# Kernel optimization log

Hardware: AMD Instinct MI355X
Metric: run time of the kernel (lower is better)

## Reference

```python
import jax, jax.numpy as jnp
import numpy as np

CAPACITY = 1024


def setup_inputs() -> dict:
    T, H, I, E, K = 2048, 1024, 1408, 8, 2
    key = jax.random.key(0)
    k0, k1, k2, k3, k4 = jax.random.split(key, 5)
    hidden_states = jax.random.normal(k0, (T, H), dtype=jnp.float32)
    w1 = jax.random.normal(k1, (E, 2 * I, H), dtype=jnp.float32) * 0.02  # [gate; up]
    w2 = jax.random.normal(k2, (E, H, I), dtype=jnp.float32) * 0.02
    topk_weights = jax.random.uniform(k3, (T, K), dtype=jnp.float32)
    topk_ids = jax.random.randint(k4, (T, K), 0, E, dtype=jnp.int32)
    return {"hidden_states": hidden_states, "w1": w1, "w2": w2,
            "topk_weights": topk_weights, "topk_ids": topk_ids}


def reference(hidden_states, w1, w2, topk_weights, topk_ids):
    # MoE: prepare(dispatch) -> grouped expert GEMM (silu-gated MLP) -> finalize(combine)
    T, H = hidden_states.shape
    E = w1.shape[0]
    I = w2.shape[2]
    K = topk_ids.shape[1]
    C = CAPACITY

    # ---- prepare: dispatch token copies to per-expert buffers ----
    flat_ids = topk_ids.reshape(-1)                       # (T*K,)
    onehot = jax.nn.one_hot(flat_ids, E, dtype=jnp.int32)  # (T*K, E)
    cs = jnp.cumsum(onehot, axis=0)                        # running per-expert counts
    pos = jnp.take_along_axis(cs, flat_ids[:, None], axis=1)[:, 0] - 1  # slot in expert buffer
    keep = pos < C
    pos_c = jnp.where(keep, pos, 0)

    x_flat = jnp.repeat(hidden_states, K, axis=0)          # (T*K, H)
    x_e = jnp.zeros((E, C, H), dtype=hidden_states.dtype)
    x_e = x_e.at[flat_ids, pos_c].add(jnp.where(keep[:, None], x_flat, 0.0))

    # ---- grouped expert GEMM: silu(gate) * up, then down-proj ----
    h = jnp.einsum('ech,eoh->eco', x_e, w1)                # (E, C, 2I)
    gate, up = h[..., :I], h[..., I:]
    act = jax.nn.silu(gate) * up                           # (E, C, I)
    y = jnp.einsum('eci,ehi->ech', act, w2)                # (E, C, H)

    # ---- finalize: gather back, apply router weights, reduce over top-k ----
    y_flat = y[flat_ids, pos_c] * (keep[:, None].astype(y.dtype)) \
             * topk_weights.reshape(-1, 1)                 # (T*K, H)
    out = y_flat.reshape(T, K, H).sum(axis=1)              # (T, H)
    return out.astype(hidden_states.dtype)
```

## Files before the change

kernel.cpp:

```cpp
#include <hip/hip_runtime.h>

#define NE 8
#define CAP 1024
#define HD 1024
#define ID 1408
#define TT 2048

typedef __attribute__((ext_vector_type(8))) short bf16x8;
typedef __attribute__((ext_vector_type(4))) float f32x4;
typedef unsigned short u16;
typedef unsigned int u32;
typedef unsigned long long u64;

__device__ __forceinline__ u16 f2bf(float f) {
  u32 u = __float_as_uint(f);
  u = (u + 0x7fffu + ((u >> 16) & 1u)) >> 16;
  return (u16)u;
}

__device__ __forceinline__ bf16x8 pack8(float4 a, float4 b) {
  bf16x8 r;
  r[0] = (short)f2bf(a.x); r[1] = (short)f2bf(a.y);
  r[2] = (short)f2bf(a.z); r[3] = (short)f2bf(a.w);
  r[4] = (short)f2bf(b.x); r[5] = (short)f2bf(b.y);
  r[6] = (short)f2bf(b.z); r[7] = (short)f2bf(b.w);
  return r;
}

__device__ __forceinline__ void async_cp16(const void* g, void* l) {
  __builtin_amdgcn_global_load_lds(
      (const __attribute__((address_space(1))) u32*)g,
      (__attribute__((address_space(3))) u32*)l, 16, 0, 0);
}

#define W1B (NE * 2 * ID / 4)
#define W2B (NE * HD * ID / 4096)
#define XB (TT * HD / 4096)
__global__ __launch_bounds__(256) void prep_kernel(
    const float4* __restrict__ w1, bf16x8* __restrict__ bw1,
    const float4* __restrict__ w2, bf16x8* __restrict__ bw2,
    const float4* __restrict__ x, bf16x8* __restrict__ bx,
    float4* __restrict__ out, const int* __restrict__ ids,
    int* __restrict__ rowmap, int* __restrict__ counts) {
  int b = blockIdx.x;
  int tid = threadIdx.x;
  if (b == 0) {
    __shared__ unsigned char ids_s[TT * 2];
    __shared__ int sc[256][NE + 1];
    for (int i = tid; i < TT * 2; i += 256) ids_s[i] = (unsigned char)ids[i];
    __syncthreads();
    int base = tid * 16;
    u64 own64 = 0;
#pragma unroll
    for (int j = 0; j < 16; ++j) own64 += 1ull << (ids_s[base + j] * 8);
    int own[NE];
#pragma unroll
    for (int e = 0; e < NE; ++e) {
      own[e] = (int)((own64 >> (e * 8)) & 0xff);
      sc[tid][e] = own[e];
    }
    __syncthreads();
    for (int off = 1; off < 256; off <<= 1) {
      int v[NE];
      if (tid >= off) {
#pragma unroll
        for (int e = 0; e < NE; ++e) v[e] = sc[tid - off][e];
      }
      __syncthreads();
      if (tid >= off) {
#pragma unroll
        for (int e = 0; e < NE; ++e) sc[tid][e] += v[e];
      }
      __syncthreads();
    }
    if (tid == 255) {
#pragma unroll
      for (int e = 0; e < NE; ++e) counts[e] = sc[255][e] < CAP ? sc[255][e] : CAP;
    }
    int excl[NE];
#pragma unroll
    for (int e = 0; e < NE; ++e) excl[e] = sc[tid][e] - own[e];
    __syncthreads();
#pragma unroll
    for (int e = 0; e < NE; ++e) sc[tid][e] = excl[e];
#pragma unroll
    for (int j = 0; j < 16; ++j) {
      int f = base + j;
      int e = ids_s[f];
      int p = sc[tid][e]++;
      if (p < CAP) rowmap[e * CAP + p] = f;
    }
    return;
  }
  int bb = b - 1;
  if (bb < W1B) {
    int rl = tid >> 6, c = tid & 63;
    int g = bb * 4 + rl;
    int e = g / (2 * ID);
    int n = g - e * (2 * ID);
    int j = (n < ID) ? n : (n - ID);
    int np = (j >> 4) * 32 + (j & 15) + ((n < ID) ? 0 : 16);
    const float4* src = w1 + ((size_t)e * 2 * ID + n) * (HD / 4);
    bf16x8* dst = bw1 + ((size_t)e * 2 * ID + np) * (HD / 8);
    float4 v0 = src[c * 2];
    float4 v1 = src[c * 2 + 1];
    float4 v2 = src[128 + c * 2];
    float4 v3 = src[128 + c * 2 + 1];
    dst[c] = pack8(v0, v1);
    dst[64 + c] = pack8(v2, v3);
  } else if (bb < W1B + W2B) {
    size_t base4 = (size_t)(bb - W1B) * 1024;
    float4 v0 = w2[base4 + tid * 2];
    float4 v1 = w2[base4 + tid * 2 + 1];
    float4 v2 = w2[base4 + 512 + tid * 2];
    float4 v3 = w2[base4 + 512 + tid * 2 + 1];
    bf16x8* dst = bw2 + base4 / 2;
    dst[tid] = pack8(v0, v1);
    dst[256 + tid] = pack8(v2, v3);
  } else {
    size_t base4 = (size_t)(bb - W1B - W2B) * 1024;
    float4 v0 = x[base4 + tid * 2];
    float4 v1 = x[base4 + tid * 2 + 1];
    float4 v2 = x[base4 + 512 + tid * 2];
    float4 v3 = x[base4 + 512 + tid * 2 + 1];
    bf16x8* dst = bx + base4 / 2;
    dst[tid] = pack8(v0, v1);
    dst[256 + tid] = pack8(v2, v3);
    float4 z = {0.f, 0.f, 0.f, 0.f};
    out[base4 + tid] = z;
    out[base4 + 256 + tid] = z;
    out[base4 + 512 + tid] = z;
    out[base4 + 768 + tid] = z;
  }
}

#define G1BUF 24576
__global__ __launch_bounds__(256) void gemm1_kernel(
    const u16* __restrict__ A, const u16* __restrict__ B, u16* __restrict__ Hb,
    const int* __restrict__ rowmap, const int* __restrict__ counts) {
  int e = blockIdx.x;
  int count = counts[e];
  int m0 = blockIdx.y * 64;
  if (m0 >= count) return;
  int n0 = blockIdx.z * 128;
  int tid = threadIdx.x;
  int lane = tid & 63, wid = tid >> 6;
  int wm = wid >> 1, wn = wid & 1;
  int q = lane >> 4, lm = lane & 15;

  __shared__ __align__(16) char sm[3 * G1BUF];

  int rloc = tid >> 3;
  int chs = ((tid & 7) ^ (rloc & 7)) * 8;
  const u16* aP[2];
  const u16* bP[4];
#pragma unroll
  for (int i = 0; i < 2; ++i) {
    int gr = m0 + rloc + 32 * i;
    int f = (gr < count) ? rowmap[e * CAP + gr] : 0;
    aP[i] = A + (size_t)(f >> 1) * HD + chs;
  }
#pragma unroll
  for (int i = 0; i < 4; ++i)
    bP[i] = B + ((size_t)e * 2 * ID + n0 + rloc + 32 * i) * HD + chs;

  f32x4 zero = {0.f, 0.f, 0.f, 0.f};
  f32x4 acc[2][4];
#pragma unroll
  for (int mi = 0; mi < 2; ++mi)
#pragma unroll
    for (int ni = 0; ni < 4; ++ni) acc[mi][ni] = zero;

#define STAGE1(base, kt)                                             \
  do {                                                               \
    int ko_ = (kt) * 64;                                             \
    char* sb_ = (base);                                              \
    async_cp16(aP[0] + ko_, sb_ + (0 * 256 + tid) * 16);             \
    async_cp16(aP[1] + ko_, sb_ + (1 * 256 + tid) * 16);             \
    async_cp16(bP[0] + ko_, sb_ + 8192 + (0 * 256 + tid) * 16);      \
    async_cp16(bP[1] + ko_, sb_ + 8192 + (1 * 256 + tid) * 16);      \
    async_cp16(bP[2] + ko_, sb_ + 8192 + (2 * 256 + tid) * 16);      \
    async_cp16(bP[3] + ko_, sb_ + 8192 + (3 * 256 + tid) * 16);      \
  } while (0)

  STAGE1(sm, 0);
  STAGE1(sm + G1BUF, 1);
  int p = 0, pn2 = 2;
  for (int kt = 0; kt < HD / 64; ++kt) {
    if (kt == HD / 64 - 1)
      asm volatile("s_waitcnt vmcnt(0)\ns_barrier" ::: "memory");
    else
      asm volatile("s_waitcnt vmcnt(6)\ns_barrier" ::: "memory");
    const char* sb = sm + p * G1BUF;
    if (kt + 2 < HD / 64) STAGE1(sm + pn2 * G1BUF, kt + 2);
#pragma unroll
    for (int s = 0; s < 2; ++s) {
      int cs = ((s * 4 + q) ^ (lm & 7)) * 16;
      bf16x8 af[2], bfr[4];
#pragma unroll
      for (int mi = 0; mi < 2; ++mi)
        af[mi] = *(const bf16x8*)(sb + (wm * 32 + mi * 16 + lm) * 128 + cs);
#pragma unroll
      for (int ni = 0; ni < 4; ++ni)
        bfr[ni] = *(const bf16x8*)(sb + 8192 + (wn * 64 + ni * 16 + lm) * 128 + cs);
      __builtin_amdgcn_s_setprio(1);
#pragma unroll
      for (int mi = 0; mi < 2; ++mi)
#pragma unroll
        for (int ni = 0; ni < 4; ++ni)
          acc[mi][ni] = __builtin_amdgcn_mfma_f32_16x16x32_bf16(af[mi], bfr[ni], acc[mi][ni], 0, 0, 0);
      __builtin_amdgcn_s_setprio(0);
    }
    p = (p == 2) ? 0 : p + 1;
    pn2 = (pn2 == 2) ? 0 : pn2 + 1;
  }
  __syncthreads();

  u16* smOut = (u16*)sm;
#pragma unroll
  for (int mi = 0; mi < 2; ++mi) {
#pragma unroll
    for (int k = 0; k < 2; ++k) {
      int colL = wn * 32 + k * 16 + lm;
#pragma unroll
      for (int r = 0; r < 4; ++r) {
        float g = acc[mi][2 * k][r];
        float u = acc[mi][2 * k + 1][r];
        float a = g / (1.f + __expf(-g)) * u;
        int row = wm * 32 + mi * 16 + q * 4 + r;
        smOut[row * 72 + colL] = f2bf(a);
      }
    }
  }
  __syncthreads();
  {
    int row = tid >> 2, seg = tid & 3;
    const u16* sp = smOut + row * 72 + seg * 16;
    bf16x8 v0 = *(const bf16x8*)sp;
    bf16x8 v1 = *(const bf16x8*)(sp + 8);
    u16* dp = Hb + ((size_t)e * CAP + m0 + row) * ID + (n0 >> 1) + seg * 16;
    *(bf16x8*)dp = v0;
    *(bf16x8*)(dp + 8) = v1;
  }
}

#define G2BUF 16384
__global__ __launch_bounds__(256) void gemm2_kernel(
    const u16* __restrict__ A, const u16* __restrict__ B, float* __restrict__ out,
    const int* __restrict__ rowmap, const int* __restrict__ counts,
    const float* __restrict__ tw) {
  int e = blockIdx.x;
  int count = counts[e];
  int m0 = blockIdx.y * 64;
  if (m0 >= count) return;
  int n0 = blockIdx.z * 64;
  int tid = threadIdx.x;
  int lane = tid & 63, wid = tid >> 6;
  int wm = wid >> 1, wn = wid & 1;
  int q = lane >> 4, lm = lane & 15;

  __shared__ __align__(16) char sm[3 * G2BUF];

  int rloc = tid >> 3;
  int chs = ((tid & 7) ^ (rloc & 7)) * 8;
  const u16* aP[2];
  const u16* bP[2];
#pragma unroll
  for (int i = 0; i < 2; ++i) {
    aP[i] = A + ((size_t)e * CAP + m0 + rloc + 32 * i) * ID + chs;
    bP[i] = B + ((size_t)e * HD + n0 + rloc + 32 * i) * ID + chs;
  }

  f32x4 zero = {0.f, 0.f, 0.f, 0.f};
  f32x4 acc[2][2];
#pragma unroll
  for (int mi = 0; mi < 2; ++mi)
#pragma unroll
    for (int ni = 0; ni < 2; ++ni) acc[mi][ni] = zero;

#define STAGE2(base, kt)                                             \
  do {                                                               \
    int ko_ = (kt) * 64;                                             \
    char* sb_ = (base);                                              \
    async_cp16(aP[0] + ko_, sb_ + (0 * 256 + tid) * 16);             \
    async_cp16(aP[1] + ko_, sb_ + (1 * 256 + tid) * 16);             \
    async_cp16(bP[0] + ko_, sb_ + 8192 + (0 * 256 + tid) * 16);      \
    async_cp16(bP[1] + ko_, sb_ + 8192 + (1 * 256 + tid) * 16);      \
  } while (0)

  STAGE2(sm, 0);
  STAGE2(sm + G2BUF, 1);
  int p = 0, pn2 = 2;
  for (int kt = 0; kt < ID / 64; ++kt) {
    if (kt == ID / 64 - 1)
      asm volatile("s_waitcnt vmcnt(0)\ns_barrier" ::: "memory");
    else
      asm volatile("s_waitcnt vmcnt(4)\ns_barrier" ::: "memory");
    const char* sb = sm + p * G2BUF;
    if (kt + 2 < ID / 64) STAGE2(sm + pn2 * G2BUF, kt + 2);
#pragma unroll
    for (int s = 0; s < 2; ++s) {
      int cs = ((s * 4 + q) ^ (lm & 7)) * 16;
      bf16x8 af[2], bfr[2];
#pragma unroll
      for (int mi = 0; mi < 2; ++mi)
        af[mi] = *(const bf16x8*)(sb + (wm * 32 + mi * 16 + lm) * 128 + cs);
#pragma unroll
      for (int ni = 0; ni < 2; ++ni)
        bfr[ni] = *(const bf16x8*)(sb + 8192 + (wn * 32 + ni * 16 + lm) * 128 + cs);
      __builtin_amdgcn_s_setprio(1);
#pragma unroll
      for (int mi = 0; mi < 2; ++mi)
#pragma unroll
        for (int ni = 0; ni < 2; ++ni)
          acc[mi][ni] = __builtin_amdgcn_mfma_f32_16x16x32_bf16(af[mi], bfr[ni], acc[mi][ni], 0, 0, 0);
      __builtin_amdgcn_s_setprio(0);
    }
    p = (p == 2) ? 0 : p + 1;
    pn2 = (pn2 == 2) ? 0 : pn2 + 1;
  }

#pragma unroll
  for (int mi = 0; mi < 2; ++mi) {
#pragma unroll
    for (int r = 0; r < 4; ++r) {
      int grow = m0 + wm * 32 + mi * 16 + q * 4 + r;
      if (grow < count) {
        int f = rowmap[e * CAP + grow];
        float w = tw[f];
        int t = f >> 1;
#pragma unroll
        for (int ni = 0; ni < 2; ++ni) {
          int col = n0 + wn * 32 + ni * 16 + lm;
          atomicAdd(&out[(size_t)t * HD + col], w * acc[mi][ni][r]);
        }
      }
    }
  }
}

extern "C" void kernel_launch(void* const* d_in, const int* in_sizes, int n_in,
                              void* d_out, int out_size, void* d_ws, size_t ws_size,
                              hipStream_t stream) {
  const float* hidden = (const float*)d_in[0];
  const float* w1 = (const float*)d_in[1];
  const float* w2 = (const float*)d_in[2];
  const float* tw = (const float*)d_in[3];
  const int* ids = (const int*)d_in[4];
  float* out = (float*)d_out;

  char* p = (char*)d_ws;
  auto alloc = [&](size_t b) { char* r = p; p += (b + 255) & ~(size_t)255; return r; };
  u16* bw1 = (u16*)alloc((size_t)NE * 2 * ID * HD * 2);
  u16* bw2 = (u16*)alloc((size_t)NE * HD * ID * 2);
  u16* bx = (u16*)alloc((size_t)TT * HD * 2);
  u16* hbuf = (u16*)alloc((size_t)NE * CAP * ID * 2);
  int* rowmap = (int*)alloc((size_t)NE * CAP * 4);
  int* counts = (int*)alloc((size_t)NE * 4);

  prep_kernel<<<1 + W1B + W2B + XB, 256, 0, stream>>>(
      (const float4*)w1, (bf16x8*)bw1, (const float4*)w2, (bf16x8*)bw2,
      (const float4*)hidden, (bf16x8*)bx, (float4*)out, ids, rowmap, counts);

  gemm1_kernel<<<dim3(NE, CAP / 64, 2 * ID / 128), 256, 0, stream>>>(
      bx, bw1, hbuf, rowmap, counts);

  gemm2_kernel<<<dim3(NE, CAP / 64, HD / 64), 256, 0, stream>>>(
      hbuf, bw2, out, rowmap, counts, tw);
}
```

Before: 262.3 us.

## Move w2 conversion and output zeroing into gemm1 launch to overlap with GEMM

The w2 fp32-to-bf16 conversion and the output zeroing move out of the prep kernel and into extra leading blocks of the gemm1 launch. That work then runs alongside the first GEMM instead of before it. The prep kernel now converts w1 and x with one row (or one 256-element chunk) per block using 4-wide stores, giving more, smaller blocks. The extra blocks in gemm1 compete with GEMM blocks for CUs, and the narrower stores in prep may lower bandwidth efficiency.

Result: faster. 256.7 us (-2.1%).

```diff
diff --git a/kernel.cpp b/kernel.cpp
--- a/kernel.cpp
+++ b/kernel.cpp
@@ -33,15 +33,13 @@
       (__attribute__((address_space(3))) u32*)l, 16, 0, 0);
 }
 
-#define W1B (NE * 2 * ID / 4)
-#define W2B (NE * HD * ID / 4096)
-#define XB (TT * HD / 4096)
+#define W1ROWS (NE * 2 * ID)
+#define XBLK (TT * HD / 4 / 256)
 __global__ __launch_bounds__(256) void prep_kernel(
-    const float4* __restrict__ w1, bf16x8* __restrict__ bw1,
-    const float4* __restrict__ w2, bf16x8* __restrict__ bw2,
-    const float4* __restrict__ x, bf16x8* __restrict__ bx,
-    float4* __restrict__ out, const int* __restrict__ ids,
-    int* __restrict__ rowmap, int* __restrict__ counts) {
+    const float4* __restrict__ w1, ushort4* __restrict__ bw1,
+    const float4* __restrict__ x, ushort4* __restrict__ bx,
+    const int* __restrict__ ids, int* __restrict__ rowmap,
+    int* __restrict__ counts) {
   int b = blockIdx.x;
   int tid = threadIdx.x;
   if (b == 0) {
@@ -93,57 +91,59 @@
     return;
   }
   int bb = b - 1;
-  if (bb < W1B) {
-    int rl = tid >> 6, c = tid & 63;
-    int g = bb * 4 + rl;
-    int e = g / (2 * ID);
-    int n = g - e * (2 * ID);
+  if (bb < W1ROWS) {
+    int n = bb % (2 * ID);
+    int e = bb / (2 * ID);
     int j = (n < ID) ? n : (n - ID);
     int np = (j >> 4) * 32 + (j & 15) + ((n < ID) ? 0 : 16);
-    const float4* src = w1 + ((size_t)e * 2 * ID + n) * (HD / 4);
-    bf16x8* dst = bw1 + ((size_t)e * 2 * ID + np) * (HD / 8);
-    float4 v0 = src[c * 2];
-    float4 v1 = src[c * 2 + 1];
-    float4 v2 = src[128 + c * 2];
-    float4 v3 = src[128 + c * 2 + 1];
-    dst[c] = pack8(v0, v1);
-    dst[64 + c] = pack8(v2, v3);
-  } else if (bb < W1B + W2B) {
-    size_t base4 = (size_t)(bb - W1B) * 1024;
-    float4 v0 = w2[base4 + tid * 2];
-    float4 v1 = w2[base4 + tid * 2 + 1];
-    float4 v2 = w2[base4 + 512 + tid * 2];
-    float4 v3 = w2[base4 + 512 + tid * 2 + 1];
-    bf16x8* dst = bw2 + base4 / 2;
-    dst[tid] = pack8(v0, v1);
-    dst[256 + tid] = pack8(v2, v3);
+    float4 v = w1[((size_t)e * 2 * ID + n) * (HD / 4) + tid];
+    ushort4 o;
+    o.x = f2bf(v.x); o.y = f2bf(v.y); o.z = f2bf(v.z); o.w = f2bf(v.w);
+    bw1[((size_t)e * 2 * ID + np) * (HD / 4) + tid] = o;
   } else {
-    size_t base4 = (size_t)(bb - W1B - W2B) * 1024;
-    float4 v0 = x[base4 + tid * 2];
-    float4 v1 = x[base4 + tid * 2 + 1];
-    float4 v2 = x[base4 + 512 + tid * 2];
-    float4 v3 = x[base4 + 512 + tid * 2 + 1];
-    bf16x8* dst = bx + base4 / 2;
-    dst[tid] = pack8(v0, v1);
-    dst[256 + tid] = pack8(v2, v3);
-    float4 z = {0.f, 0.f, 0.f, 0.f};
-    out[base4 + tid] = z;
-    out[base4 + 256 + tid] = z;
-    out[base4 + 512 + tid] = z;
-    out[base4 + 768 + tid] = z;
+    size_t i = (size_t)(bb - W1ROWS) * 256 + tid;
+    float4 v = x[i];
+    ushort4 o;
+    o.x = f2bf(v.x); o.y = f2bf(v.y); o.z = f2bf(v.z); o.w = f2bf(v.w);
+    bx[i] = o;
   }
 }
 
 #define G1BUF 24576
 __global__ __launch_bounds__(256) void gemm1_kernel(
     const u16* __restrict__ A, const u16* __restrict__ B, u16* __restrict__ Hb,
-    const int* __restrict__ rowmap, const int* __restrict__ counts) {
-  int e = blockIdx.x;
+    const int* __restrict__ rowmap, const int* __restrict__ counts,
+    const float4* __restrict__ W2, bf16x8* __restrict__ bw2,
+    float4* __restrict__ outz) {
+  int bid = blockIdx.x;
+  int tid = threadIdx.x;
+  if (bid < 704) {
+#pragma unroll
+    for (int k2 = 0; k2 < 4; ++k2) {
+      size_t base4 = ((size_t)bid * 4 + k2) * 1024;
+      float4 v0 = W2[base4 + tid * 2];
+      float4 v1 = W2[base4 + tid * 2 + 1];
+      float4 v2 = W2[base4 + 512 + tid * 2];
+      float4 v3 = W2[base4 + 512 + tid * 2 + 1];
+      bf16x8* dst = bw2 + base4 / 2;
+      dst[tid] = pack8(v0, v1);
+      dst[256 + tid] = pack8(v2, v3);
+    }
+    return;
+  }
+  if (bid < 768) {
+    size_t base = (size_t)(bid - 704) * 8192;
+    float4 z = {0.f, 0.f, 0.f, 0.f};
+#pragma unroll
+    for (int i2 = 0; i2 < 32; ++i2) outz[base + i2 * 256 + tid] = z;
+    return;
+  }
+  int g = bid - 768;
+  int e = g & 7;
+  int m0 = ((g >> 3) & 15) * 64;
+  int n0 = (g >> 7) * 128;
   int count = counts[e];
-  int m0 = blockIdx.y * 64;
   if (m0 >= count) return;
-  int n0 = blockIdx.z * 128;
-  int tid = threadIdx.x;
   int lane = tid & 63, wid = tid >> 6;
   int wm = wid >> 1, wn = wid & 1;
   int q = lane >> 4, lm = lane & 15;
@@ -224,9 +224,9 @@
       int colL = wn * 32 + k * 16 + lm;
 #pragma unroll
       for (int r = 0; r < 4; ++r) {
-        float g = acc[mi][2 * k][r];
+        float g2 = acc[mi][2 * k][r];
         float u = acc[mi][2 * k + 1][r];
-        float a = g / (1.f + __expf(-g)) * u;
+        float a = g2 / (1.f + __expf(-g2)) * u;
         int row = wm * 32 + mi * 16 + q * 4 + r;
         smOut[row * 72 + colL] = f2bf(a);
       }
@@ -358,12 +358,13 @@
   int* rowmap = (int*)alloc((size_t)NE * CAP * 4);
   int* counts = (int*)alloc((size_t)NE * 4);
 
-  prep_kernel<<<1 + W1B + W2B + XB, 256, 0, stream>>>(
-      (const float4*)w1, (bf16x8*)bw1, (const float4*)w2, (bf16x8*)bw2,
-      (const float4*)hidden, (bf16x8*)bx, (float4*)out, ids, rowmap, counts);
-
-  gemm1_kernel<<<dim3(NE, CAP / 64, 2 * ID / 128), 256, 0, stream>>>(
-      bx, bw1, hbuf, rowmap, counts);
+  prep_kernel<<<1 + W1ROWS + XBLK, 256, 0, stream>>>(
+      (const float4*)w1, (ushort4*)bw1, (const float4*)hidden, (ushort4*)bx,
+      ids, rowmap, counts);
+
+  gemm1_kernel<<<768 + NE * (CAP / 64) * (2 * ID / 128), 256, 0, stream>>>(
+      bx, bw1, hbuf, rowmap, counts, (const float4*)w2, (bf16x8*)bw2,
+      (float4*)out);
 
   gemm2_kernel<<<dim3(NE, CAP / 64, HD / 64), 256, 0, stream>>>(
       hbuf, bw2, out, rowmap, counts, tw);
```
